# Performance work log

Hardware: AMD Instinct MI355X
Metric: run time of the kernel (lower is better)

Reference implementation:

```python
import jax, jax.numpy as jnp
import numpy as np

EPS = 1e-12

def _wn(v, g):
    # weight norm per output channel (axis 0): w[o] = g[o] * v[o] / ||v[o]||
    return g[:, None] * v / jnp.linalg.norm(v, axis=1, keepdims=True)

def _unit(x):
    # row-wise L2 normalize with clip, matching _normalize in source
    return x / jnp.clip(jnp.linalg.norm(x, axis=-1, keepdims=True), EPS)

def setup_inputs() -> dict:
    key = jax.random.key(0)
    ks = jax.random.split(key, 8)
    D, CD, K, T = 1024, 256, 8192, 16384
    return {
        "z": jax.random.normal(ks[0], (D, T), dtype=jnp.float32),
        "in_v": jax.random.normal(ks[1], (CD, D), dtype=jnp.float32) * 0.02,
        "in_g": jax.random.uniform(ks[2], (CD,), dtype=jnp.float32, minval=0.5, maxval=1.5),
        "in_b": jax.random.normal(ks[3], (CD,), dtype=jnp.float32) * 0.01,
        "out_v": jax.random.normal(ks[4], (D, CD), dtype=jnp.float32) * 0.02,
        "out_g": jax.random.uniform(ks[5], (D,), dtype=jnp.float32, minval=0.5, maxval=1.5),
        "out_b": jax.random.normal(ks[6], (D,), dtype=jnp.float32) * 0.01,
        "codebook": jax.random.normal(ks[7], (K, CD), dtype=jnp.float32),
    }

def reference(z, in_v, in_g, in_b, out_v, out_g, out_b, codebook):
    # in_proj: weight-normed 1x1 conv == matmul over channel dim
    z_e = _wn(in_v, in_g) @ z + in_b[:, None]            # (CD, T)
    # decode_latents
    enc = _unit(z_e.T)                                    # (T, CD)
    cb = _unit(codebook)                                  # (K, CD)
    # squared L2 distance via matmul-based cdist
    dist = (jnp.sum(enc * enc, axis=1, keepdims=True)
            - 2.0 * enc @ cb.T
            + jnp.sum(cb * cb, axis=1)[None, :])          # (T, K)
    indices = jnp.argmax(-dist, axis=1)                   # (T,)
    z_q = codebook[indices].T                             # (CD, T), raw codebook gather
    # straight-through estimator
    z_q = z_e + jax.lax.stop_gradient(z_q - z_e)
    # out_proj
    out = _wn(out_v, out_g) @ z_q + out_b[:, None]        # (D, T)
    return (out, indices)
```

## Files before the change

kernel.cpp:

```cpp
#include <hip/hip_runtime.h>
#include <hip/hip_bf16.h>
#include <math.h>

#define TDIM 16384
#define DDIM 1024
#define CDIM 256
#define KDIM 8192
#define KSPLIT 8

typedef unsigned short u16;
typedef __attribute__((ext_vector_type(8))) short bf16x8;
typedef __attribute__((ext_vector_type(8))) unsigned short us8;
typedef __attribute__((ext_vector_type(4))) float floatx4;

static const size_t OFF_WINH  = 0;
static const size_t OFF_WINL  = OFF_WINH  + (size_t)CDIM * DDIM / 2;
static const size_t OFF_WOUTH = OFF_WINL  + (size_t)CDIM * DDIM / 2;
static const size_t OFF_WOUTL = OFF_WOUTH + (size_t)DDIM * CDIM / 2;
static const size_t OFF_CBH   = OFF_WOUTL + (size_t)DDIM * CDIM / 2;
static const size_t OFF_CBL   = OFF_CBH   + (size_t)KDIM * CDIM / 2;
static const size_t OFF_C2    = OFF_CBL   + (size_t)KDIM * CDIM / 2;
static const size_t OFF_ZTH   = OFF_C2    + (size_t)KDIM;
static const size_t OFF_ZTL   = OFF_ZTH   + (size_t)TDIM * DDIM / 2;
static const size_t OFF_ZE    = OFF_ZTL   + (size_t)TDIM * DDIM / 2;
static const size_t OFF_PV    = OFF_ZE    + (size_t)CDIM * TDIM;
static const size_t OFF_PI    = OFF_PV    + (size_t)KSPLIT * TDIM;
static const size_t OFF_IDX   = OFF_PI    + (size_t)KSPLIT * TDIM;
static const size_t OFF_ETH   = OFF_ZTH;
static const size_t OFF_ETL   = OFF_ZTH + (size_t)TDIM * CDIM / 2;

static __device__ __forceinline__ u16 f2bf(float x) {
  __hip_bfloat16 h = __float2bfloat16(x);
  return *(u16*)&h;
}
static __device__ __forceinline__ float bf2f(u16 u) {
  __hip_bfloat16 h; *(u16*)&h = u;
  return __bfloat162float(h);
}

static __device__ __forceinline__ void gload16(const u16* g, u16* l) {
  __builtin_amdgcn_global_load_lds(
      (__attribute__((address_space(1))) void*)g,
      (__attribute__((address_space(3))) void*)l, 16, 0, 0);
}

__global__ __launch_bounds__(256) void rownorm_split(
    const float* __restrict__ v, const float* __restrict__ g,
    u16* __restrict__ hi, u16* __restrict__ lo, float* __restrict__ c2,
    int ncols, int clip) {
  __shared__ float red[256];
  int row = blockIdx.x;
  const float* vr = v + (size_t)row * ncols;
  float s = 0.f;
  for (int j = threadIdx.x; j < ncols; j += 256) { float x = vr[j]; s += x * x; }
  red[threadIdx.x] = s;
  __syncthreads();
  for (int off = 128; off > 0; off >>= 1) {
    if (threadIdx.x < off) red[threadIdx.x] += red[threadIdx.x + off];
    __syncthreads();
  }
  float norm = sqrtf(red[0]);
  if (clip) norm = fmaxf(norm, 1e-12f);
  float scale = (g ? g[row] : 1.0f) / norm;
  float s2 = 0.f;
  for (int j = threadIdx.x; j < ncols; j += 256) {
    float y = vr[j] * scale;
    u16 hh = f2bf(y);
    u16 ll = f2bf(y - bf2f(hh));
    hi[(size_t)row * ncols + j] = hh;
    lo[(size_t)row * ncols + j] = ll;
    s2 += y * y;
  }
  if (c2) {
    __syncthreads();
    red[threadIdx.x] = s2;
    __syncthreads();
    for (int off = 128; off > 0; off >>= 1) {
      if (threadIdx.x < off) red[threadIdx.x] += red[threadIdx.x + off];
      __syncthreads();
    }
    if (threadIdx.x == 0) c2[row] = red[0];
  }
}

__global__ __launch_bounds__(256) void transpose_split_z(
    const float* __restrict__ z, u16* __restrict__ zth, u16* __restrict__ ztl) {
  __shared__ float tile[64][65];
  int t0 = blockIdx.x * 64, d0 = blockIdx.y * 64;
  int tl = threadIdx.x & 63, grp = threadIdx.x >> 6;
#pragma unroll
  for (int r = 0; r < 16; r++) {
    int d = grp * 16 + r;
    tile[d][tl] = z[(size_t)(d0 + d) * TDIM + t0 + tl];
  }
  __syncthreads();
#pragma unroll
  for (int r = 0; r < 16; r++) {
    int t = grp * 16 + r;
    float x = tile[tl][t];
    u16 h = f2bf(x);
    u16 l = f2bf(x - bf2f(h));
    zth[(size_t)(t0 + t) * DDIM + d0 + tl] = h;
    ztl[(size_t)(t0 + t) * DDIM + d0 + tl] = l;
  }
}

__global__ __launch_bounds__(256) void gemm_mfma_in(
    const u16* __restrict__ ah_g, const u16* __restrict__ al_g,
    const u16* __restrict__ bh_g, const u16* __restrict__ bl_g,
    const float* __restrict__ bias, float* __restrict__ C, int K) {
  __shared__ u16 Ah[128 * 32], Al[128 * 32];
  __shared__ u16 Bh[64 * 32],  Bl[64 * 32];
  int tid = threadIdx.x;
  int n0 = blockIdx.x * 64;
  int m0 = blockIdx.y * 128;
  int lane = tid & 63, wid = tid >> 6;
  int wr = wid >> 1, wc = wid & 1;
  int q = lane >> 4, mm = lane & 15;
  int h = tid & 1;
  int sr = ((tid >> 1) ^ (h << 2)) & 127;
  int ssw = (sr ^ (sr >> 2)) & 3;
  int o0 = sr * 32 + ((((h << 1))     ^ ssw) << 3);
  int o1 = sr * 32 + ((((h << 1) | 1) ^ ssw) << 3);
  int gcol = h * 16;
  int sb = ((tid >> 1) ^ (h << 2)) & 63;
  int ssb = (sb ^ (sb >> 2)) & 3;
  int p0 = sb * 32 + ((((h << 1))     ^ ssb) << 3);
  int p1 = sb * 32 + ((((h << 1) | 1) ^ ssb) << 3);
  int sm = (mm ^ (mm >> 2)) & 3;
  int cq = (q ^ sm) << 3;

  const floatx4 z4 = {0.f, 0.f, 0.f, 0.f};
  floatx4 acc[4][2];
#pragma unroll
  for (int i = 0; i < 4; i++)
#pragma unroll
    for (int j = 0; j < 2; j++) acc[i][j] = z4;

  for (int c0 = 0; c0 < K; c0 += 32) {
    const size_t ga = (size_t)(m0 + sr) * K + c0 + gcol;
    us8 a_h0 = *(const us8*)&ah_g[ga];
    us8 a_h1 = *(const us8*)&ah_g[ga + 8];
    us8 a_l0 = *(const us8*)&al_g[ga];
    us8 a_l1 = *(const us8*)&al_g[ga + 8];
    us8 b_h0, b_h1, b_l0, b_l1;
    if (tid < 128) {
      const size_t gb = (size_t)(n0 + sb) * K + c0 + gcol;
      b_h0 = *(const us8*)&bh_g[gb];
      b_h1 = *(const us8*)&bh_g[gb + 8];
      b_l0 = *(const us8*)&bl_g[gb];
      b_l1 = *(const us8*)&bl_g[gb + 8];
    }
    __syncthreads();
    *(us8*)&Ah[o0] = a_h0; *(us8*)&Ah[o1] = a_h1;
    *(us8*)&Al[o0] = a_l0; *(us8*)&Al[o1] = a_l1;
    if (tid < 128) {
      *(us8*)&Bh[p0] = b_h0; *(us8*)&Bh[p1] = b_h1;
      *(us8*)&Bl[p0] = b_l0; *(us8*)&Bl[p1] = b_l1;
    }
    __syncthreads();

    bf16x8 fa[4], fb[2];
#pragma unroll
    for (int i = 0; i < 4; i++)
      fa[i] = *(const bf16x8*)&Ah[(wr * 64 + i * 16 + mm) * 32 + cq];
#pragma unroll
    for (int j = 0; j < 2; j++)
      fb[j] = *(const bf16x8*)&Bh[(wc * 32 + j * 16 + mm) * 32 + cq];
#pragma unroll
    for (int i = 0; i < 4; i++)
#pragma unroll
      for (int j = 0; j < 2; j++)
        acc[i][j] = __builtin_amdgcn_mfma_f32_16x16x32_bf16(fa[i], fb[j], acc[i][j], 0, 0, 0);
#pragma unroll
    for (int i = 0; i < 4; i++) {
      bf16x8 fl = *(const bf16x8*)&Al[(wr * 64 + i * 16 + mm) * 32 + cq];
#pragma unroll
      for (int j = 0; j < 2; j++)
        acc[i][j] = __builtin_amdgcn_mfma_f32_16x16x32_bf16(fl, fb[j], acc[i][j], 0, 0, 0);
    }
#pragma unroll
    for (int j = 0; j < 2; j++) {
      bf16x8 fl = *(const bf16x8*)&Bl[(wc * 32 + j * 16 + mm) * 32 + cq];
#pragma unroll
      for (int i = 0; i < 4; i++)
        acc[i][j] = __builtin_amdgcn_mfma_f32_16x16x32_bf16(fa[i], fl, acc[i][j], 0, 0, 0);
    }
  }

#pragma unroll
  for (int i = 0; i < 4; i++) {
#pragma unroll
    for (int r = 0; r < 4; r++) {
      int m_loc = wr * 64 + i * 16 + q * 4 + r;
      float bb = bias[m0 + m_loc];
      float* crow = &C[(size_t)(m0 + m_loc) * TDIM + n0 + wc * 32 + mm];
#pragma unroll
      for (int j = 0; j < 2; j++) crow[j * 16] = acc[i][j][r] + bb;
    }
  }
}

__global__ __launch_bounds__(256) void gemm_mfma_bias(
    const u16* __restrict__ ah_g, const u16* __restrict__ al_g,
    const u16* __restrict__ bh_g, const u16* __restrict__ bl_g,
    const float* __restrict__ bias, float* __restrict__ C, int K) {
  __shared__ u16 Ah[128 * 32], Al[128 * 32];
  __shared__ u16 Bh[128 * 32], Bl[128 * 32];
  int tid = threadIdx.x;
  int n0 = blockIdx.x * 128;
  int m0 = blockIdx.y * 128;
  int lane = tid & 63, wid = tid >> 6;
  int wr = wid >> 1, wc = wid & 1;
  int q = lane >> 4, mm = lane & 15;
  int h = tid & 1;
  int sr = ((tid >> 1) ^ (h << 2)) & 127;
  int ssw = (sr ^ (sr >> 2)) & 3;
  int o0 = sr * 32 + ((((h << 1))     ^ ssw) << 3);
  int o1 = sr * 32 + ((((h << 1) | 1) ^ ssw) << 3);
  int gcol = h * 16;
  int sm = (mm ^ (mm >> 2)) & 3;
  int cq = (q ^ sm) << 3;

  const floatx4 z4 = {0.f, 0.f, 0.f, 0.f};
  floatx4 acc[4][4];
#pragma unroll
  for (int i = 0; i < 4; i++)
#pragma unroll
    for (int j = 0; j < 4; j++) acc[i][j] = z4;

  for (int c0 = 0; c0 < K; c0 += 32) {
    const size_t ga = (size_t)(m0 + sr) * K + c0 + gcol;
    const size_t gb = (size_t)(n0 + sr) * K + c0 + gcol;
    us8 a_h0 = *(const us8*)&ah_g[ga];
    us8 a_h1 = *(const us8*)&ah_g[ga + 8];
    us8 a_l0 = *(const us8*)&al_g[ga];
    us8 a_l1 = *(const us8*)&al_g[ga + 8];
    us8 b_h0 = *(const us8*)&bh_g[gb];
    us8 b_h1 = *(const us8*)&bh_g[gb + 8];
    us8 b_l0 = *(const us8*)&bl_g[gb];
    us8 b_l1 = *(const us8*)&bl_g[gb + 8];
    __syncthreads();
    *(us8*)&Ah[o0] = a_h0; *(us8*)&Ah[o1] = a_h1;
    *(us8*)&Al[o0] = a_l0; *(us8*)&Al[o1] = a_l1;
    *(us8*)&Bh[o0] = b_h0; *(us8*)&Bh[o1] = b_h1;
    *(us8*)&Bl[o0] = b_l0; *(us8*)&Bl[o1] = b_l1;
    __syncthreads();

    bf16x8 fa[4], fb[4];
#pragma unroll
    for (int i = 0; i < 4; i++)
      fa[i] = *(const bf16x8*)&Ah[(wr * 64 + i * 16 + mm) * 32 + cq];
#pragma unroll
    for (int j = 0; j < 4; j++)
      fb[j] = *(const bf16x8*)&Bh[(wc * 64 + j * 16 + mm) * 32 + cq];
#pragma unroll
    for (int i = 0; i < 4; i++)
#pragma unroll
      for (int j = 0; j < 4; j++)
        acc[i][j] = __builtin_amdgcn_mfma_f32_16x16x32_bf16(fa[i], fb[j], acc[i][j], 0, 0, 0);
#pragma unroll
    for (int i = 0; i < 4; i++) {
      bf16x8 fl = *(const bf16x8*)&Al[(wr * 64 + i * 16 + mm) * 32 + cq];
#pragma unroll
      for (int j = 0; j < 4; j++)
        acc[i][j] = __builtin_amdgcn_mfma_f32_16x16x32_bf16(fl, fb[j], acc[i][j], 0, 0, 0);
    }
#pragma unroll
    for (int j = 0; j < 4; j++) {
      bf16x8 fl = *(const bf16x8*)&Bl[(wc * 64 + j * 16 + mm) * 32 + cq];
#pragma unroll
      for (int i = 0; i < 4; i++)
        acc[i][j] = __builtin_amdgcn_mfma_f32_16x16x32_bf16(fa[i], fl, acc[i][j], 0, 0, 0);
    }
  }

#pragma unroll
  for (int i = 0; i < 4; i++) {
#pragma unroll
    for (int r = 0; r < 4; r++) {
      int m_loc = wr * 64 + i * 16 + q * 4 + r;
      float bb = bias[m0 + m_loc];
      float* crow = &C[(size_t)(m0 + m_loc) * TDIM + n0 + wc * 64 + mm];
#pragma unroll
      for (int j = 0; j < 4; j++) crow[j * 16] = acc[i][j][r] + bb;
    }
  }
}

__global__ __launch_bounds__(256) void finish_ze(
    const float* __restrict__ ze, u16* __restrict__ eth, u16* __restrict__ etl) {
  __shared__ float tile[256][33];
  __shared__ float red[8][32];
  __shared__ float invs[32];
  int t0 = blockIdx.x * 32;
  int tl = threadIdx.x & 31, grp = threadIdx.x >> 5;
  float s = 0.f;
  for (int c = grp * 32; c < grp * 32 + 32; c++) {
    float v = ze[(size_t)c * TDIM + t0 + tl];
    tile[c][tl] = v;
    s += v * v;
  }
  red[grp][tl] = s;
  __syncthreads();
  if (grp == 0) {
    float tot = 0.f;
#pragma unroll
    for (int gg = 0; gg < 8; gg++) tot += red[gg][tl];
    invs[tl] = 1.0f / fmaxf(sqrtf(tot), 1e-12f);
  }
  __syncthreads();
#pragma unroll
  for (int r = 0; r < 4; r++) {
    int t = grp * 4 + r;
    float iv = invs[t];
#pragma unroll
    for (int cc = 0; cc < 8; cc++) {
      int cd = cc * 32 + tl;
      float x = tile[cd][t] * iv;
      u16 hh = f2bf(x);
      u16 ll = f2bf(x - bf2f(hh));
      eth[(size_t)(t0 + t) * CDIM + cd] = hh;
      etl[(size_t)(t0 + t) * CDIM + cd] = ll;
    }
  }
}

__global__ __launch_bounds__(512, 2) void dist_mfma(
    const u16* __restrict__ eth, const u16* __restrict__ etl,
    const u16* __restrict__ cbh, const u16* __restrict__ cbl,
    const float* __restrict__ c2, float* __restrict__ pv, int* __restrict__ pi) {
  __shared__ u16 BhL[128 * 256];
  __shared__ u16 AhL[2][128 * 64];
  __shared__ u16 AlL[2][128 * 64];
  __shared__ float mv[2][128];
  __shared__ int   mi[2][128];

  int tid = threadIdx.x;
  int t0 = blockIdx.x * 128;
  int kbeg = blockIdx.y * (KDIM / KSPLIT);
  int lane = tid & 63, wid = tid >> 6;
  int wk = wid >> 2, wt = wid & 3;
  int q = lane >> 4, mm = lane & 15;

  int stR[2], stC[2], stL[2];
#pragma unroll
  for (int it = 0; it < 2; it++) {
    int gi = it * 512 + tid;
    int r = gi >> 3, g = gi & 7;
    stR[it] = r;
    stC[it] = (g ^ (r & 7)) << 3;
    stL[it] = gi << 3;
  }

  int foff[2];
#pragma unroll
  for (int kk = 0; kk < 2; kk++)
    foff[kk] = ((((kk << 2) | q) ^ (mm & 7)) << 3);

#pragma unroll
  for (int it = 0; it < 8; ++it) {
    int gi = it * 512 + tid;
    int r = gi >> 5, p = gi & 31;
    gload16(&eth[(size_t)(t0 + r) * CDIM + ((p ^ (r & 7)) << 3)], &BhL[gi << 3]);
  }
  bf16x8 fbl[2][8];
#pragma unroll
  for (int j = 0; j < 2; ++j)
#pragma unroll
    for (int sl = 0; sl < 8; ++sl)
      fbl[j][sl] = *(const bf16x8*)
          &etl[(size_t)(t0 + wt * 32 + j * 16 + mm) * CDIM + sl * 32 + q * 8];
#pragma unroll
  for (int it = 0; it < 2; ++it) {
    const size_t ga = (size_t)(kbeg + stR[it]) * CDIM + stC[it];
    gload16(&cbh[ga], &AhL[0][stL[it]]);
    gload16(&cbl[ga], &AlL[0][stL[it]]);
  }

  float rbv[2]; int rbi[2];
#pragma unroll
  for (int j = 0; j < 2; j++) { rbv[j] = INFINITY; rbi[j] = 0x7fffffff; }

  const floatx4 z4 = {0.f, 0.f, 0.f, 0.f};
  floatx4 acc[4][2];
#pragma unroll
  for (int i = 0; i < 4; i++)
#pragma unroll
    for (int j = 0; j < 2; j++) acc[i][j] = z4;

  for (int ks = 0; ks < 8; ++ks) {
#pragma unroll
    for (int cc = 0; cc < 4; ++cc) {
      const int b = cc & 1;
      __syncthreads();

      int nglob = ks * 4 + cc;
      if (nglob < 31) {
        int n1 = nglob + 1;
        int k0n = kbeg + (n1 >> 2) * 128;
        int c0n = (n1 & 3) * 64;
#pragma unroll
        for (int it = 0; it < 2; ++it) {
          const size_t ga = (size_t)(k0n + stR[it]) * CDIM + c0n + stC[it];
          gload16(&cbh[ga], &AhL[b ^ 1][stL[it]]);
          gload16(&cbl[ga], &AlL[b ^ 1][stL[it]]);
        }
      }

#pragma unroll
      for (int kk = 0; kk < 2; ++kk) {
        bf16x8 fah[4], fbh[2];
#pragma unroll
        for (int i = 0; i < 4; i++)
          fah[i] = *(const bf16x8*)&AhL[b][(wk * 64 + i * 16 + mm) * 64 + foff[kk]];
#pragma unroll
        for (int j = 0; j < 2; j++)
          fbh[j] = *(const bf16x8*)&BhL[(wt * 32 + j * 16 + mm) * 256 +
                                        (((cc * 8 + kk * 4 + q) ^ (mm & 7)) << 3)];
#pragma unroll
        for (int i = 0; i < 4; i++)
#pragma unroll
          for (int j = 0; j < 2; j++)
            acc[i][j] = __builtin_amdgcn_mfma_f32_16x16x32_bf16(fah[i], fbh[j], acc[i][j], 0, 0, 0);
#pragma unroll
        for (int i = 0; i < 4; i++) {
          bf16x8 fl = *(const bf16x8*)&AlL[b][(wk * 64 + i * 16 + mm) * 64 + foff[kk]];
#pragma unroll
          for (int j = 0; j < 2; j++)
            acc[i][j] = __builtin_amdgcn_mfma_f32_16x16x32_bf16(fl, fbh[j], acc[i][j], 0, 0, 0);
        }
#pragma unroll
        for (int j = 0; j < 2; j++) {
#pragma unroll
          for (int i = 0; i < 4; i++)
            acc[i][j] = __builtin_amdgcn_mfma_f32_16x16x32_bf16(fah[i], fbl[j][cc * 2 + kk], acc[i][j], 0, 0, 0);
        }
      }
    }

    int k0 = kbeg + ks * 128;
#pragma unroll
    for (int i = 0; i < 4; i++) {
#pragma unroll
      for (int r4 = 0; r4 < 4; r4++) {
        int kg = k0 + wk * 64 + i * 16 + q * 4 + r4;
        float c2v = c2[kg];
#pragma unroll
        for (int j = 0; j < 2; j++) {
          float s = c2v - 2.0f * acc[i][j][r4];
          if (s < rbv[j]) { rbv[j] = s; rbi[j] = kg; }
        }
      }
    }
#pragma unroll
    for (int i = 0; i < 4; i++)
#pragma unroll
      for (int j = 0; j < 2; j++) acc[i][j] = z4;
  }

#pragma unroll
  for (int j = 0; j < 2; j++) {
    float v = rbv[j]; int ii = rbi[j];
    float ov = __shfl_xor(v, 16, 64); int oi = __shfl_xor(ii, 16, 64);
    if (ov < v || (ov == v && oi < ii)) { v = ov; ii = oi; }
    ov = __shfl_xor(v, 32, 64); oi = __shfl_xor(ii, 32, 64);
    if (ov < v || (ov == v && oi < ii)) { v = ov; ii = oi; }
    rbv[j] = v; rbi[j] = ii;
  }
  __syncthreads();
  if (q == 0) {
#pragma unroll
    for (int j = 0; j < 2; j++) {
      mv[wk][wt * 32 + j * 16 + mm] = rbv[j];
      mi[wk][wt * 32 + j * 16 + mm] = rbi[j];
    }
  }
  __syncthreads();
  if (tid < 128) {
    float v0 = mv[0][tid]; int i0 = mi[0][tid];
    float v1 = mv[1][tid]; int i1 = mi[1][tid];
    if (v1 < v0 || (v1 == v0 && i1 < i0)) { v0 = v1; i0 = i1; }
    pv[(size_t)blockIdx.y * TDIM + t0 + tid] = v0;
    pi[(size_t)blockIdx.y * TDIM + t0 + tid] = i0;
  }
}

__global__ __launch_bounds__(256) void merge_argmin(
    const float* __restrict__ pv, const int* __restrict__ pi,
    int* __restrict__ idx, float* __restrict__ idxf) {
  int t = blockIdx.x * 256 + threadIdx.x;
  float bv = INFINITY; int bi = 0x7fffffff;
  for (int s = 0; s < KSPLIT; s++) {
    float v = pv[(size_t)s * TDIM + t];
    int ii = pi[(size_t)s * TDIM + t];
    if (v < bv || (v == bv && ii < bi)) { bv = v; bi = ii; }
  }
  idx[t] = bi;
  idxf[t] = (float)bi;
}

__global__ __launch_bounds__(256) void gather_split(
    const int* __restrict__ idx, const float* __restrict__ cb,
    u16* __restrict__ zqh, u16* __restrict__ zql) {
  int t = blockIdx.x * 4 + (threadIdx.x >> 6);
  int c4 = (threadIdx.x & 63) * 4;
  int k = idx[t];
  float4 x = *(const float4*)&cb[(size_t)k * CDIM + c4];
  u16 h0 = f2bf(x.x), h1 = f2bf(x.y), h2 = f2bf(x.z), h3 = f2bf(x.w);
  u16 l0 = f2bf(x.x - bf2f(h0)), l1 = f2bf(x.y - bf2f(h1));
  u16 l2 = f2bf(x.z - bf2f(h2)), l3 = f2bf(x.w - bf2f(h3));
  ushort4 hv = {h0, h1, h2, h3}, lv = {l0, l1, l2, l3};
  *(ushort4*)&zqh[(size_t)t * CDIM + c4] = hv;
  *(ushort4*)&zql[(size_t)t * CDIM + c4] = lv;
}

extern "C" void kernel_launch(void* const* d_in, const int* in_sizes, int n_in,
                              void* d_out, int out_size, void* d_ws, size_t ws_size,
                              hipStream_t stream) {
  const float* z     = (const float*)d_in[0];
  const float* in_v  = (const float*)d_in[1];
  const float* in_g  = (const float*)d_in[2];
  const float* in_b  = (const float*)d_in[3];
  const float* out_v = (const float*)d_in[4];
  const float* out_g = (const float*)d_in[5];
  const float* out_b = (const float*)d_in[6];
  const float* cb    = (const float*)d_in[7];

  float* ws    = (float*)d_ws;
  u16*   winh  = (u16*)(ws + OFF_WINH);
  u16*   winl  = (u16*)(ws + OFF_WINL);
  u16*   wouth = (u16*)(ws + OFF_WOUTH);
  u16*   woutl = (u16*)(ws + OFF_WOUTL);
  u16*   cbh   = (u16*)(ws + OFF_CBH);
  u16*   cbl   = (u16*)(ws + OFF_CBL);
  float* c2    = ws + OFF_C2;
  u16*   zth   = (u16*)(ws + OFF_ZTH);
  u16*   ztl   = (u16*)(ws + OFF_ZTL);
  float* z_e   = ws + OFF_ZE;
  float* pv    = ws + OFF_PV;
  int*   pi    = (int*)(ws + OFF_PI);
  int*   idxw  = (int*)(ws + OFF_IDX);
  u16*   eth   = (u16*)(ws + OFF_ETH);
  u16*   etl   = (u16*)(ws + OFF_ETL);
  u16*   zqh   = eth;
  u16*   zql   = etl;

  float* outp = (float*)d_out;
  float* idxf = outp + (size_t)DDIM * TDIM;

  rownorm_split<<<CDIM, 256, 0, stream>>>(in_v, in_g, winh, winl, nullptr, DDIM, 0);
  rownorm_split<<<DDIM, 256, 0, stream>>>(out_v, out_g, wouth, woutl, nullptr, CDIM, 0);
  rownorm_split<<<KDIM, 256, 0, stream>>>(cb, nullptr, cbh, cbl, c2, CDIM, 1);

  transpose_split_z<<<dim3(TDIM / 64, DDIM / 64), 256, 0, stream>>>(z, zth, ztl);

  gemm_mfma_in<<<dim3(TDIM / 64, CDIM / 128), 256, 0, stream>>>(
      winh, winl, zth, ztl, in_b, z_e, DDIM);

  finish_ze<<<TDIM / 32, 256, 0, stream>>>(z_e, eth, etl);

  dist_mfma<<<dim3(TDIM / 128, KSPLIT), 512, 0, stream>>>(eth, etl, cbh, cbl, c2, pv, pi);
  merge_argmin<<<TDIM / 256, 256, 0, stream>>>(pv, pi, idxw, idxf);

  gather_split<<<TDIM / 4, 256, 0, stream>>>(idxw, cb, zqh, zql);

  gemm_mfma_bias<<<dim3(TDIM / 128, DDIM / 128), 256, 0, stream>>>(
      wouth, woutl, zqh, zql, out_b, outp, CDIM);
}
```

Measured before the change: 434.5 us.

## Hold encoder tiles in registers and deepen codebook LDS pipeline to four stages

The dist_mfma kernel now loads both the hi and lo encoder fragments straight into registers, so the large shared-memory B tile goes away. The freed LDS is spent on a 4-stage ring buffer of codebook chunks with three loads in flight, gated by vmcnt waits and raw s_barrier in place of __syncthreads. The block's c2 norms are staged in LDS, and s_setprio is raised around the MFMA bursts. The aim is to hide global-load latency and cut LDS traffic, at the cost of more registers (fbh and fbl arrays) and fragile manual waitcnt/barrier correctness; the wrap-around prefetch also issues redundant loads on the last iterations.

```diff
diff --git a/kernel.cpp b/kernel.cpp
--- a/kernel.cpp
+++ b/kernel.cpp
@@ -330,9 +330,9 @@
     const u16* __restrict__ eth, const u16* __restrict__ etl,
     const u16* __restrict__ cbh, const u16* __restrict__ cbl,
     const float* __restrict__ c2, float* __restrict__ pv, int* __restrict__ pi) {
-  __shared__ u16 BhL[128 * 256];
-  __shared__ u16 AhL[2][128 * 64];
-  __shared__ u16 AlL[2][128 * 64];
+  __shared__ u16 AhL[4][128 * 64];
+  __shared__ u16 AlL[4][128 * 64];
+  __shared__ float c2L[1024];
   __shared__ float mv[2][128];
   __shared__ int   mi[2][128];
 
@@ -358,25 +358,27 @@
   for (int kk = 0; kk < 2; kk++)
     foff[kk] = ((((kk << 2) | q) ^ (mm & 7)) << 3);
 
-#pragma unroll
-  for (int it = 0; it < 8; ++it) {
-    int gi = it * 512 + tid;
-    int r = gi >> 5, p = gi & 31;
-    gload16(&eth[(size_t)(t0 + r) * CDIM + ((p ^ (r & 7)) << 3)], &BhL[gi << 3]);
-  }
-  bf16x8 fbl[2][8];
+  float2 c2v2 = *(const float2*)&c2[kbeg + tid * 2];
+  bf16x8 fbh[2][8], fbl[2][8];
 #pragma unroll
   for (int j = 0; j < 2; ++j)
 #pragma unroll
-    for (int sl = 0; sl < 8; ++sl)
-      fbl[j][sl] = *(const bf16x8*)
-          &etl[(size_t)(t0 + wt * 32 + j * 16 + mm) * CDIM + sl * 32 + q * 8];
-#pragma unroll
-  for (int it = 0; it < 2; ++it) {
-    const size_t ga = (size_t)(kbeg + stR[it]) * CDIM + stC[it];
-    gload16(&cbh[ga], &AhL[0][stL[it]]);
-    gload16(&cbl[ga], &AlL[0][stL[it]]);
-  }
+    for (int sl = 0; sl < 8; ++sl) {
+      const size_t gb = (size_t)(t0 + wt * 32 + j * 16 + mm) * CDIM + sl * 32 + q * 8;
+      fbh[j][sl] = *(const bf16x8*)&eth[gb];
+      fbl[j][sl] = *(const bf16x8*)&etl[gb];
+    }
+  *(float2*)&c2L[tid * 2] = c2v2;
+#pragma unroll
+  for (int p = 0; p < 3; ++p) {
+#pragma unroll
+    for (int it = 0; it < 2; ++it) {
+      const size_t ga = (size_t)(kbeg + stR[it]) * CDIM + p * 64 + stC[it];
+      gload16(&cbh[ga], &AhL[p][stL[it]]);
+      gload16(&cbl[ga], &AlL[p][stL[it]]);
+    }
+  }
+  asm volatile("s_waitcnt lgkmcnt(0)" ::: "memory");
 
   float rbv[2]; int rbi[2];
 #pragma unroll
@@ -392,43 +394,41 @@
   for (int ks = 0; ks < 8; ++ks) {
 #pragma unroll
     for (int cc = 0; cc < 4; ++cc) {
-      const int b = cc & 1;
-      __syncthreads();
-
-      int nglob = ks * 4 + cc;
-      if (nglob < 31) {
-        int n1 = nglob + 1;
-        int k0n = kbeg + (n1 >> 2) * 128;
-        int c0n = (n1 & 3) * 64;
+      asm volatile("s_waitcnt vmcnt(8)" ::: "memory");
+      __builtin_amdgcn_s_barrier();
+      __builtin_amdgcn_sched_barrier(0);
+
+      {
+        int nn = (ks * 4 + cc + 3) & 31;
+        int k0n = kbeg + ((nn >> 2) * 128);
+        const int c0n = ((cc + 3) & 3) * 64;
+        const int nb = (cc + 3) & 3;
 #pragma unroll
         for (int it = 0; it < 2; ++it) {
           const size_t ga = (size_t)(k0n + stR[it]) * CDIM + c0n + stC[it];
-          gload16(&cbh[ga], &AhL[b ^ 1][stL[it]]);
-          gload16(&cbl[ga], &AlL[b ^ 1][stL[it]]);
+          gload16(&cbh[ga], &AhL[nb][stL[it]]);
+          gload16(&cbl[ga], &AlL[nb][stL[it]]);
         }
       }
 
+      __builtin_amdgcn_s_setprio(1);
 #pragma unroll
       for (int kk = 0; kk < 2; ++kk) {
-        bf16x8 fah[4], fbh[2];
+        bf16x8 fah[4];
 #pragma unroll
         for (int i = 0; i < 4; i++)
-          fah[i] = *(const bf16x8*)&AhL[b][(wk * 64 + i * 16 + mm) * 64 + foff[kk]];
-#pragma unroll
-        for (int j = 0; j < 2; j++)
-          fbh[j] = *(const bf16x8*)&BhL[(wt * 32 + j * 16 + mm) * 256 +
-                                        (((cc * 8 + kk * 4 + q) ^ (mm & 7)) << 3)];
+          fah[i] = *(const bf16x8*)&AhL[cc][(wk * 64 + i * 16 + mm) * 64 + foff[kk]];
 #pragma unroll
         for (int i = 0; i < 4; i++)
 #pragma unroll
           for (int j = 0; j < 2; j++)
-            acc[i][j] = __builtin_amdgcn_mfma_f32_16x16x32_bf16(fah[i], fbh[j], acc[i][j], 0, 0, 0);
+            acc[i][j] = __builtin_amdgcn_mfma_f32_16x16x32_bf16(fah[i], fbh[j][cc * 2 + kk], acc[i][j], 0, 0, 0);
 #pragma unroll
         for (int i = 0; i < 4; i++) {
-          bf16x8 fl = *(const bf16x8*)&AlL[b][(wk * 64 + i * 16 + mm) * 64 + foff[kk]];
+          bf16x8 fl = *(const bf16x8*)&AlL[cc][(wk * 64 + i * 16 + mm) * 64 + foff[kk]];
 #pragma unroll
           for (int j = 0; j < 2; j++)
-            acc[i][j] = __builtin_amdgcn_mfma_f32_16x16x32_bf16(fl, fbh[j], acc[i][j], 0, 0, 0);
+            acc[i][j] = __builtin_amdgcn_mfma_f32_16x16x32_bf16(fl, fbh[j][cc * 2 + kk], acc[i][j], 0, 0, 0);
         }
 #pragma unroll
         for (int j = 0; j < 2; j++) {
@@ -437,15 +437,16 @@
             acc[i][j] = __builtin_amdgcn_mfma_f32_16x16x32_bf16(fah[i], fbl[j][cc * 2 + kk], acc[i][j], 0, 0, 0);
         }
       }
-    }
-
-    int k0 = kbeg + ks * 128;
+      __builtin_amdgcn_s_setprio(0);
+    }
+
 #pragma unroll
     for (int i = 0; i < 4; i++) {
+      floatx4 cv = *(const floatx4*)&c2L[ks * 128 + wk * 64 + i * 16 + q * 4];
 #pragma unroll
       for (int r4 = 0; r4 < 4; r4++) {
-        int kg = k0 + wk * 64 + i * 16 + q * 4 + r4;
-        float c2v = c2[kg];
+        int kg = kbeg + ks * 128 + wk * 64 + i * 16 + q * 4 + r4;
+        float c2v = cv[r4];
 #pragma unroll
         for (int j = 0; j < 2; j++) {
           float s = c2v - 2.0f * acc[i][j][r4];
@@ -468,7 +469,6 @@
     if (ov < v || (ov == v && oi < ii)) { v = ov; ii = oi; }
     rbv[j] = v; rbi[j] = ii;
   }
-  __syncthreads();
   if (q == 0) {
 #pragma unroll
     for (int j = 0; j < 2; j++) {
```

New measurement: 432.7 us. About the same (-0.4%).
